# Kernel optimization log

Measured on AMD Instinct MI355X. Metric: run time of the kernel, lower is better.

The kernel has to match this reference:

```python
import jax, jax.numpy as jnp
import numpy as np

B, C, H, W = 16, 256, 56, 56
K = 7            # involution kernel size
GC = 16          # group_channels
G = C // GC      # groups = 16
RED = C // 4     # reduction_ratio = 4
EPS = 1e-5
PAD = (K - 1) // 2


def _bn(x, g, b, m, v):
    # eval-mode BatchNorm2d over channel dim of (B,C,H,W)
    scale = g / jnp.sqrt(v + EPS)
    return x * scale[:, None, None] + (b - m * scale)[:, None, None]


def _conv1x1(x, w, b):
    # x: (B,Cin,H,W), w: (Cout,Cin)
    return jnp.einsum('bchw,oc->bohw', x, w) + b[None, :, None, None]


def setup_inputs() -> dict:
    key = jax.random.key(0)
    ks = jax.random.split(key, 32)
    def n(i, shape, s=0.05):
        return jax.random.normal(ks[i], shape, jnp.float32) * s
    return {
        'x': jax.random.normal(ks[0], (B, C, H, W), jnp.float32),
        'w1': n(1, (C, C)), 'b1': n(2, (C,)),
        'bn1_g': 1.0 + n(3, (C,)), 'bn1_b': n(4, (C,)),
        'bn1_m': n(5, (C,)), 'bn1_v': 1.0 + 0.1 * jax.random.uniform(ks[6], (C,)),
        'red_w': n(7, (RED, C)), 'red_b': n(8, (RED,)),
        'red_bn_g': 1.0 + n(9, (RED,)), 'red_bn_b': n(10, (RED,)),
        'red_bn_m': n(11, (RED,)), 'red_bn_v': 1.0 + 0.1 * jax.random.uniform(ks[12], (RED,)),
        'span_w': n(13, (K * K * G, RED)), 'span_b': n(14, (K * K * G,)),
        'bn2_g': 1.0 + n(15, (C,)), 'bn2_b': n(16, (C,)),
        'bn2_m': n(17, (C,)), 'bn2_v': 1.0 + 0.1 * jax.random.uniform(ks[18], (C,)),
        'w3': n(19, (C, C)), 'b3': n(20, (C,)),
        'bn3_g': 1.0 + n(21, (C,)), 'bn3_b': n(22, (C,)),
        'bn3_m': n(23, (C,)), 'bn3_v': 1.0 + 0.1 * jax.random.uniform(ks[24], (C,)),
    }


def _involution(y, red_w, red_b, rg, rb, rm, rv, span_w, span_b):
    # dynamic per-pixel kernels: (B, G, K*K, H, W)
    r = jax.nn.relu(_bn(_conv1x1(y, red_w, red_b), rg, rb, rm, rv))
    wd = _conv1x1(r, span_w, span_b).reshape(B, G, K * K, H, W)
    # pad input once; accumulate over the K*K shifted views (no unfold copy)
    yp = jnp.pad(y, ((0, 0), (0, 0), (PAD, PAD), (PAD, PAD)))
    yp = yp.reshape(B, G, GC, H + 2 * PAD, W + 2 * PAD)
    out = jnp.zeros((B, G, GC, H, W), y.dtype)
    for i in range(K):
        for j in range(K):
            out = out + wd[:, :, i * K + j, None] * yp[:, :, :, i:i + H, j:j + W]
    return out.reshape(B, C, H, W)


def reference(x, w1, b1, bn1_g, bn1_b, bn1_m, bn1_v,
              red_w, red_b, red_bn_g, red_bn_b, red_bn_m, red_bn_v,
              span_w, span_b, bn2_g, bn2_b, bn2_m, bn2_v,
              w3, b3, bn3_g, bn3_b, bn3_m, bn3_v):
    y = jnp.tanh(_bn(_conv1x1(x, w1, b1), bn1_g, bn1_b, bn1_m, bn1_v))
    y = _involution(y, red_w, red_b, red_bn_g, red_bn_b, red_bn_m, red_bn_v, span_w, span_b)
    y = jnp.tanh(_bn(y, bn2_g, bn2_b, bn2_m, bn2_v))
    y = _bn(_conv1x1(y, w3, b3), bn3_g, bn3_b, bn3_m, bn3_v)
    return y + x  # use_skip: inv_stride==1 and input_dim==output_dim
```

## Files before the change

### kernel.cpp

```cpp
#include <hip/hip_runtime.h>
#include <math.h>

#define DEV_EPS 1e-5f

namespace {
constexpr int B_ = 16, C_ = 256, H_ = 56, W_ = 56, HW_ = H_ * W_;
constexpr int G_ = 16, GC_ = 16, RED_ = 64, KK_ = 49;
constexpr int NTOT = B_ * HW_;

typedef __attribute__((ext_vector_type(8))) short short8;
typedef __attribute__((ext_vector_type(4))) float f32x4;

__device__ __forceinline__ unsigned short bf16r(float f) {
  unsigned u = __float_as_uint(f);
  u += 0x7fff + ((u >> 16) & 1);
  return (unsigned short)(u >> 16);
}
__device__ __forceinline__ float bf2f(unsigned short s) {
  return __uint_as_float((unsigned)s << 16);
}

__device__ __forceinline__ float fast_tanh(float x) {
  float ax = fabsf(x);
  float e = __expf(-2.0f * ax);
  float r = (1.0f - e) * __builtin_amdgcn_rcpf(1.0f + e);
  return copysignf(r, x);
}

__device__ __forceinline__ void gl_lds16(const void* g, void* l) {
  __builtin_amdgcn_global_load_lds(
      (const __attribute__((address_space(1))) unsigned int*)g,
      (__attribute__((address_space(3))) unsigned int*)l, 16, 0, 0);
}

template <int WM, int WN, int KD, int EPI>
__global__ __launch_bounds__(256)
void mfma_gemm(const unsigned short* __restrict__ A,
               const unsigned short* __restrict__ Act,
               const float* __restrict__ p0,
               const float* __restrict__ bg, const float* __restrict__ bb,
               const float* __restrict__ bm, const float* __restrict__ bv,
               const float* __restrict__ xskip, void* __restrict__ outp,
               int M) {
  constexpr int BM = WM * 64, BN = WN * 64;
  __shared__ unsigned short At[BM * 64];
  __shared__ unsigned short Bt[BN * 64];
  __shared__ float aS[BM], bS[BM];

  const int tid = threadIdx.x;
  const int n0 = blockIdx.x * BN, m0 = blockIdx.y * BM;
  const int wave = tid >> 6, lane = tid & 63;
  const int wm = (WM == 2) ? (wave >> 1) : 0;
  const int wn = (WM == 2) ? (wave & 1) : wave;

  if (tid < BM) {
    int m = min(m0 + tid, M - 1);
    float sc = bg[m] * rsqrtf(bv[m] + DEV_EPS);
    aS[tid] = sc;
    bS[tid] = sc * p0[m] + bb[m] - bm[m] * sc;
  }

  f32x4 acc[4][4];
#pragma unroll
  for (int i = 0; i < 4; ++i)
#pragma unroll
    for (int j = 0; j < 4; ++j)
#pragma unroll
      for (int e = 0; e < 4; ++e) acc[i][j][e] = 0.f;

  const int lq = lane & 7;
  const int lr8 = lane >> 3;
  const int quad = lane >> 4, ln = lane & 15;

#pragma unroll 1
  for (int kt = 0; kt < KD / 64; ++kt) {
    __syncthreads();
#pragma unroll
    for (int t = 0; t < BM / 32; ++t) {
      int inst = wave * (BM / 32) + t;
      int row = inst * 8 + lr8;
      int mrow = min(m0 + row, M - 1);
      int qs = lq ^ (row & 7);
      gl_lds16(A + (size_t)mrow * KD + kt * 64 + qs * 8, &At[inst * 512]);
    }
#pragma unroll
    for (int t = 0; t < BN / 32; ++t) {
      int inst = wave * (BN / 32) + t;
      int row = inst * 8 + lr8;
      int qs = lq ^ (row & 7);
      gl_lds16(Act + (size_t)(n0 + row) * KD + kt * 64 + qs * 8, &Bt[inst * 512]);
    }
    __syncthreads();

#pragma unroll
    for (int s = 0; s < 2; ++s) {
      const int c = s * 4 + quad;
      short8 af[4], bf[4];
#pragma unroll
      for (int i = 0; i < 4; ++i) {
        int r = wm * 64 + i * 16 + ln;
        af[i] = *(const short8*)&At[r * 64 + (c ^ (r & 7)) * 8];
      }
#pragma unroll
      for (int j = 0; j < 4; ++j) {
        int r = wn * 64 + j * 16 + ln;
        bf[j] = *(const short8*)&Bt[r * 64 + (c ^ (r & 7)) * 8];
      }
#pragma unroll
      for (int i = 0; i < 4; ++i)
#pragma unroll
        for (int j = 0; j < 4; ++j)
          acc[i][j] = __builtin_amdgcn_mfma_f32_16x16x32_bf16(af[i], bf[j],
                                                              acc[i][j], 0, 0, 0);
    }
  }

#pragma unroll
  for (int i = 0; i < 4; ++i) {
    const int mloc = wm * 64 + i * 16 + quad * 4;
#pragma unroll
    for (int j = 0; j < 4; ++j) {
      const int np = n0 + wn * 64 + j * 16 + ln;
      if (EPI == 0 || EPI == 1) {
        ushort4 pk;
        unsigned short* pp = (unsigned short*)&pk;
#pragma unroll
        for (int r = 0; r < 4; ++r) {
          float v = aS[mloc + r] * acc[i][j][r] + bS[mloc + r];
          v = (EPI == 0) ? fast_tanh(v) : fmaxf(v, 0.f);
          pp[r] = bf16r(v);
        }
        *(ushort4*)((unsigned short*)outp + (size_t)np * M + m0 + mloc) = pk;
      } else {
        int b = np / HW_, hw = np - b * HW_;
        size_t base = ((size_t)b * C_ + m0 + mloc) * HW_ + hw;
#pragma unroll
        for (int r = 0; r < 4; ++r) {
          size_t o = base + (size_t)r * HW_;
          ((float*)outp)[o] =
              aS[mloc + r] * acc[i][j][r] + bS[mloc + r] + xskip[o];
        }
      }
    }
  }
}

constexpr int YS_STR = 264;

__global__ __launch_bounds__(256)
void gemm_yr(const unsigned short* __restrict__ A,
             const unsigned short* __restrict__ Act,
             const unsigned short* __restrict__ redw,
             const float* __restrict__ p0,
             const float* __restrict__ bg, const float* __restrict__ bb,
             const float* __restrict__ bm, const float* __restrict__ bv,
             const float* __restrict__ rp0,
             const float* __restrict__ rbg, const float* __restrict__ rbb,
             const float* __restrict__ rbm, const float* __restrict__ rbv,
             unsigned short* __restrict__ yT, unsigned short* __restrict__ rT) {
  constexpr int BM = 256, BN = 64;
  __shared__ __align__(16) unsigned short blob2[BM * 64 + BN * 64];
  __shared__ float aS[256], bS[256], aR[64], bR[64];
  unsigned short* At = blob2;
  unsigned short* Bt = blob2 + BM * 64;
  unsigned short* yS = blob2;

  const int tid = threadIdx.x;
  const int n0 = blockIdx.x * BN;
  const int wave = tid >> 6, lane = tid & 63;
  const int lq = lane & 7, lr8 = lane >> 3;
  const int quad = lane >> 4, ln = lane & 15;

  {
    float sc = bg[tid] * rsqrtf(bv[tid] + DEV_EPS);
    aS[tid] = sc;
    bS[tid] = sc * p0[tid] + bb[tid] - bm[tid] * sc;
    if (tid < 64) {
      float s2 = rbg[tid] * rsqrtf(rbv[tid] + DEV_EPS);
      aR[tid] = s2;
      bR[tid] = s2 * rp0[tid] + rbb[tid] - rbm[tid] * s2;
    }
  }

  f32x4 acc[4][4];
#pragma unroll
  for (int i = 0; i < 4; ++i)
#pragma unroll
    for (int j = 0; j < 4; ++j)
#pragma unroll
      for (int e = 0; e < 4; ++e) acc[i][j][e] = 0.f;

#pragma unroll 1
  for (int kt = 0; kt < 4; ++kt) {
    __syncthreads();
#pragma unroll
    for (int t = 0; t < 8; ++t) {
      int inst = wave * 8 + t;
      int row = inst * 8 + lr8;
      int qs = lq ^ (row & 7);
      gl_lds16(A + (size_t)row * 256 + kt * 64 + qs * 8, &At[inst * 512]);
    }
#pragma unroll
    for (int t = 0; t < 2; ++t) {
      int inst = wave * 2 + t;
      int row = inst * 8 + lr8;
      int qs = lq ^ (row & 7);
      gl_lds16(Act + (size_t)(n0 + row) * 256 + kt * 64 + qs * 8,
               &Bt[inst * 512]);
    }
    __syncthreads();

#pragma unroll
    for (int s = 0; s < 2; ++s) {
      const int c = s * 4 + quad;
      short8 af[4], bf[4];
#pragma unroll
      for (int i = 0; i < 4; ++i) {
        int r = wave * 64 + i * 16 + ln;
        af[i] = *(const short8*)&At[r * 64 + (c ^ (r & 7)) * 8];
      }
#pragma unroll
      for (int j = 0; j < 4; ++j) {
        int r = j * 16 + ln;
        bf[j] = *(const short8*)&Bt[r * 64 + (c ^ (r & 7)) * 8];
      }
#pragma unroll
      for (int i = 0; i < 4; ++i)
#pragma unroll
        for (int j = 0; j < 4; ++j)
          acc[i][j] = __builtin_amdgcn_mfma_f32_16x16x32_bf16(af[i], bf[j],
                                                              acc[i][j], 0, 0, 0);
    }
  }

  __syncthreads();

#pragma unroll
  for (int i = 0; i < 4; ++i) {
    const int mloc = wave * 64 + i * 16 + quad * 4;
#pragma unroll
    for (int j = 0; j < 4; ++j) {
      const int npl = j * 16 + ln;
      ushort4 pk;
      unsigned short* pp = (unsigned short*)&pk;
#pragma unroll
      for (int r = 0; r < 4; ++r) {
        float v = aS[mloc + r] * acc[i][j][r] + bS[mloc + r];
        pp[r] = bf16r(fast_tanh(v));
      }
      *(ushort4*)(yT + (size_t)(n0 + npl) * 256 + mloc) = pk;
      *(ushort4*)(yS + npl * YS_STR + mloc) = pk;
    }
  }
  __syncthreads();

  f32x4 acc2[4];
#pragma unroll
  for (int j = 0; j < 4; ++j)
#pragma unroll
    for (int e = 0; e < 4; ++e) acc2[j][e] = 0.f;
#pragma unroll
  for (int kc = 0; kc < 8; ++kc) {
    short8 af2 =
        *(const short8*)&redw[(size_t)(wave * 16 + ln) * 256 + kc * 32 + quad * 8];
#pragma unroll
    for (int j = 0; j < 4; ++j) {
      short8 bf2 = *(const short8*)&yS[(j * 16 + ln) * YS_STR + kc * 32 + quad * 8];
      acc2[j] = __builtin_amdgcn_mfma_f32_16x16x32_bf16(af2, bf2, acc2[j], 0, 0, 0);
    }
  }
  {
    const int m2 = wave * 16 + quad * 4;
#pragma unroll
    for (int j = 0; j < 4; ++j) {
      const int np = n0 + j * 16 + ln;
      ushort4 pk;
      unsigned short* pp = (unsigned short*)&pk;
#pragma unroll
      for (int r = 0; r < 4; ++r) {
        float v = aR[m2 + r] * acc2[j][r] + bR[m2 + r];
        pp[r] = bf16r(fmaxf(v, 0.f));
      }
      *(ushort4*)(rT + (size_t)np * 64 + m2) = pk;
    }
  }
}

__global__ __launch_bounds__(256)
void transpose_x(const float* __restrict__ x, unsigned short* __restrict__ xT) {
  __shared__ unsigned short tile[128 * 72];
  const int tid = threadIdx.x;
  const int px0 = blockIdx.x * 128;
  for (int p = 0; p < 4; ++p) {
    if (p) __syncthreads();
#pragma unroll
    for (int e = 0; e < 32; ++e) {
      int flat = e * 256 + tid;
      int cl = flat >> 7, pxl = flat & 127;
      int px = px0 + pxl;
      int b = px / HW_, hw = px - b * HW_;
      tile[pxl * 72 + cl] = bf16r(x[((size_t)b * C_ + p * 64 + cl) * HW_ + hw]);
    }
    __syncthreads();
    int px = tid >> 1, half = tid & 1;
    const unsigned short* src = &tile[px * 72 + half * 32];
    unsigned short* dst = &xT[(size_t)(px0 + px) * C_ + p * 64 + half * 32];
    *(uint4*)(dst + 0) = *(const uint4*)(src + 0);
    *(uint4*)(dst + 8) = *(const uint4*)(src + 8);
    *(uint4*)(dst + 16) = *(const uint4*)(src + 16);
    *(uint4*)(dst + 24) = *(const uint4*)(src + 24);
  }
}

__global__ __launch_bounds__(256)
void wconv(const float* __restrict__ w1, const float* __restrict__ rw,
           const float* __restrict__ sw, const float* __restrict__ w3,
           unsigned short* __restrict__ o1, unsigned short* __restrict__ orw,
           unsigned short* __restrict__ osw, unsigned short* __restrict__ ow3) {
  int i = blockIdx.x * 256 + threadIdx.x;
  if (i < 65536) o1[i] = bf16r(w1[i]);
  if (i < 16384) orw[i] = bf16r(rw[i]);
  if (i < 50176) osw[i] = bf16r(sw[i]);
  if (i < 65536) ow3[i] = bf16r(w3[i]);
}

constexpr int PB_STR = 648;
constexpr int W_TAP_STR = 232;
constexpr int BLOB_N = 25320;

__global__ __launch_bounds__(256)
void gather_inv(const unsigned short* __restrict__ yT,
                const unsigned short* __restrict__ rT,
                const unsigned short* __restrict__ spanw,
                const float* __restrict__ spanb,
                const float* __restrict__ g2, const float* __restrict__ b2,
                const float* __restrict__ m2, const float* __restrict__ v2,
                unsigned short* __restrict__ tT) {
  __shared__ __align__(16) unsigned short blob[BLOB_N];
  __shared__ float a2s[16], b2s[16], sbs[KK_];

  unsigned short* rs = blob;
  unsigned short* sws = blob + 14336;
  unsigned short* patchb = blob;
  unsigned short* wts = blob + 10368;
  unsigned short* tb = blob + 21736;

  const int tid = threadIdx.x;
  const int g = blockIdx.x;
  const int st = blockIdx.y;
  const int b = blockIdx.z;
  const int h0 = st * 4;
  const int wave = tid >> 6, lane = tid & 63;
  const int lq = lane & 7, lr8 = lane >> 3;
  const int quad = lane >> 4, ln = lane & 15;

  uint4 pv0[3], pv1[3];
  int poff[3];
  bool pok[3];
#pragma unroll
  for (int pi = 0; pi < 3; ++pi) {
    int e = tid + pi * 256;
    bool ok = e < 620;
    int row = e / 62, cw = e - row * 62;
    int sr = h0 + row - 3, sc = cw - 3;
    poff[pi] = row * 64 + cw;
    pok[pi] = ok;
    bool inb = ok && sr >= 0 && sr < H_ && sc >= 0 && sc < W_;
    if (inb) {
      const unsigned short* yp =
          yT + ((size_t)b * HW_ + sr * W_ + sc) * C_ + g * GC_;
      pv0[pi] = *(const uint4*)yp;
      pv1[pi] = *(const uint4*)(yp + 8);
    } else {
      pv0[pi] = make_uint4(0, 0, 0, 0);
      pv1[pi] = make_uint4(0, 0, 0, 0);
    }
  }

  {
    const unsigned short* rbase = rT + ((size_t)b * HW_ + h0 * W_) * RED_;
#pragma unroll
    for (int t = 0; t < 7; ++t) {
      int inst = wave * 7 + t;
      int row = inst * 8 + lr8;
      int qs = lq ^ (row & 7);
      gl_lds16(rbase + (size_t)row * RED_ + qs * 8, &rs[inst * 512]);
    }
    const unsigned short* swg = spanw + (size_t)(g * KK_) * RED_;
#pragma unroll
    for (int t = 0; t < 2; ++t) {
      int inst = wave * 2 + t;
      int row = inst * 8 + lr8;
      int tap = min(row, KK_ - 1);
      int qs = lq ^ (row & 7);
      gl_lds16(swg + (size_t)tap * RED_ + qs * 8, &sws[inst * 512]);
    }
    if (tid < 16) {
      int c = g * GC_ + tid;
      float sc = g2[c] * rsqrtf(v2[c] + DEV_EPS);
      a2s[tid] = sc;
      b2s[tid] = b2[c] - m2[c] * sc;
    }
    if (tid < KK_) sbs[tid] = spanb[g * KK_ + tid];
  }
  __syncthreads();

  f32x4 wacc[14];
#pragma unroll
  for (int j = 0; j < 14; ++j)
#pragma unroll
    for (int e = 0; e < 4; ++e) wacc[j][e] = 0.f;
  {
    short8 af[2];
#pragma unroll
    for (int s = 0; s < 2; ++s) {
      int c = s * 4 + quad;
      int r = wave * 16 + ln;
      af[s] = *(const short8*)&sws[r * 64 + (c ^ (r & 7)) * 8];
    }
#pragma unroll
    for (int j = 0; j < 14; ++j) {
#pragma unroll
      for (int s = 0; s < 2; ++s) {
        int c = s * 4 + quad;
        int r = j * 16 + ln;
        short8 bf = *(const short8*)&rs[r * 64 + (c ^ (r & 7)) * 8];
        wacc[j] = __builtin_amdgcn_mfma_f32_16x16x32_bf16(af[s], bf, wacc[j],
                                                          0, 0, 0);
      }
    }
  }
  __syncthreads();

  {
#pragma unroll
    for (int r = 0; r < 4; ++r) {
      int tap = wave * 16 + quad * 4 + r;
      if (tap < KK_) {
        float sb = sbs[tap];
#pragma unroll
        for (int j = 0; j < 14; ++j)
          wts[tap * W_TAP_STR + j * 16 + ln] = bf16r(wacc[j][r] + sb);
      }
    }
#pragma unroll
    for (int pi = 0; pi < 3; ++pi) {
      if (pok[pi]) {
        int off = poff[pi];
        unsigned wv[8] = {pv0[pi].x, pv0[pi].y, pv0[pi].z, pv0[pi].w,
                          pv1[pi].x, pv1[pi].y, pv1[pi].z, pv1[pi].w};
#pragma unroll
        for (int cc = 0; cc < 8; ++cc) {
          patchb[(2 * cc) * PB_STR + off] = (unsigned short)wv[cc];
          patchb[(2 * cc + 1) * PB_STR + off] = (unsigned short)(wv[cc] >> 16);
        }
      }
    }
  }
  __syncthreads();

#pragma unroll 1
  for (int it = 0; it < 2; ++it) {
    int item = tid + it * 256;
    if (item < 56 * 8) {
      const int gcp = item & 7, s = item >> 3;
      const int gc0 = gcp * 2;
      const int r0 = s / 14, c0 = (s - r0 * 14) * 4;
      const unsigned short* pg0 = patchb + gc0 * PB_STR + r0 * 64 + c0;
      const unsigned short* pg1 = pg0 + PB_STR;
      const unsigned short* wp = wts + (r0 * 56 + c0);
      float a00 = 0.f, a01 = 0.f, a02 = 0.f, a03 = 0.f;
      float a10 = 0.f, a11 = 0.f, a12 = 0.f, a13 = 0.f;
#pragma unroll
      for (int di = 0; di < 7; ++di) {
        const unsigned short* p0p = pg0 + di * 64;
        const unsigned short* p1p = pg1 + di * 64;
        uint2 q0 = *(const uint2*)p0p;
        uint2 q1 = *(const uint2*)(p0p + 4);
        uint2 q2 = *(const uint2*)(p0p + 8);
        uint2 u0 = *(const uint2*)p1p;
        uint2 u1 = *(const uint2*)(p1p + 4);
        uint2 u2 = *(const uint2*)(p1p + 8);
        unsigned uu0[6] = {q0.x, q0.y, q1.x, q1.y, q2.x, q2.y};
        unsigned uu1[6] = {u0.x, u0.y, u1.x, u1.y, u2.x, u2.y};
        float pf0[12], pf1[12];
#pragma unroll
        for (int k = 0; k < 6; ++k) {
          pf0[2 * k] = __uint_as_float(uu0[k] << 16);
          pf0[2 * k + 1] = __uint_as_float(uu0[k] & 0xffff0000u);
          pf1[2 * k] = __uint_as_float(uu1[k] << 16);
          pf1[2 * k + 1] = __uint_as_float(uu1[k] & 0xffff0000u);
        }
#pragma unroll
        for (int dj = 0; dj < 7; ++dj) {
          ushort4 wv = *(const ushort4*)(wp + (di * 7 + dj) * W_TAP_STR);
          float w0 = bf2f(wv.x), w1 = bf2f(wv.y), w2 = bf2f(wv.z),
                w3 = bf2f(wv.w);
          a00 += w0 * pf0[dj + 0];
          a01 += w1 * pf0[dj + 1];
          a02 += w2 * pf0[dj + 2];
          a03 += w3 * pf0[dj + 3];
          a10 += w0 * pf1[dj + 0];
          a11 += w1 * pf1[dj + 1];
          a12 += w2 * pf1[dj + 2];
          a13 += w3 * pf1[dj + 3];
        }
      }
      const int pxb = r0 * 56 + c0;
      {
        const float al = a2s[gc0], be = b2s[gc0];
        tb[(pxb + 0) * 16 + gc0] = bf16r(fast_tanh(al * a00 + be));
        tb[(pxb + 1) * 16 + gc0] = bf16r(fast_tanh(al * a01 + be));
        tb[(pxb + 2) * 16 + gc0] = bf16r(fast_tanh(al * a02 + be));
        tb[(pxb + 3) * 16 + gc0] = bf16r(fast_tanh(al * a03 + be));
      }
      {
        const float al = a2s[gc0 + 1], be = b2s[gc0 + 1];
        tb[(pxb + 0) * 16 + gc0 + 1] = bf16r(fast_tanh(al * a10 + be));
        tb[(pxb + 1) * 16 + gc0 + 1] = bf16r(fast_tanh(al * a11 + be));
        tb[(pxb + 2) * 16 + gc0 + 1] = bf16r(fast_tanh(al * a12 + be));
        tb[(pxb + 3) * 16 + gc0 + 1] = bf16r(fast_tanh(al * a13 + be));
      }
    }
  }
  __syncthreads();

  if (tid < 224) {
    unsigned short* dst = tT + ((size_t)b * HW_ + h0 * W_ + tid) * C_ + g * GC_;
    *(uint4*)(dst + 0) = *(const uint4*)&tb[tid * 16];
    *(uint4*)(dst + 8) = *(const uint4*)&tb[tid * 16 + 8];
  }
}

}

extern "C" void kernel_launch(void* const* d_in, const int* in_sizes, int n_in,
                              void* d_out, int out_size, void* d_ws, size_t ws_size,
                              hipStream_t stream) {
  const float* x = (const float*)d_in[0];
  const float* w1 = (const float*)d_in[1];
  const float* b1 = (const float*)d_in[2];
  const float* bn1g = (const float*)d_in[3];
  const float* bn1b = (const float*)d_in[4];
  const float* bn1m = (const float*)d_in[5];
  const float* bn1v = (const float*)d_in[6];
  const float* red_w = (const float*)d_in[7];
  const float* red_b = (const float*)d_in[8];
  const float* rbg = (const float*)d_in[9];
  const float* rbb = (const float*)d_in[10];
  const float* rbm = (const float*)d_in[11];
  const float* rbv = (const float*)d_in[12];
  const float* span_w = (const float*)d_in[13];
  const float* span_b = (const float*)d_in[14];
  const float* bn2g = (const float*)d_in[15];
  const float* bn2b = (const float*)d_in[16];
  const float* bn2m = (const float*)d_in[17];
  const float* bn2v = (const float*)d_in[18];
  const float* w3 = (const float*)d_in[19];
  const float* b3 = (const float*)d_in[20];
  const float* bn3g = (const float*)d_in[21];
  const float* bn3b = (const float*)d_in[22];
  const float* bn3m = (const float*)d_in[23];
  const float* bn3v = (const float*)d_in[24];

  unsigned short* ws = (unsigned short*)d_ws;
  unsigned short* xT = ws;
  unsigned short* yT = xT + (size_t)NTOT * C_;
  unsigned short* rT = yT + (size_t)NTOT * C_;
  unsigned short* tT = rT + (size_t)NTOT * RED_;
  unsigned short* w1b = tT + (size_t)NTOT * C_;
  unsigned short* redb = w1b + 65536;
  unsigned short* spanb = redb + 16384;
  unsigned short* w3b = spanb + 50176;
  float* out = (float*)d_out;

  dim3 blk(256);
  wconv<<<dim3(256), blk, 0, stream>>>(w1, red_w, span_w, w3, w1b, redb, spanb, w3b);
  transpose_x<<<dim3(392), blk, 0, stream>>>(x, xT);
  gemm_yr<<<dim3(784), blk, 0, stream>>>(
      w1b, xT, redb, b1, bn1g, bn1b, bn1m, bn1v,
      red_b, rbg, rbb, rbm, rbv, yT, rT);
  gather_inv<<<dim3(16, 14, 16), blk, 0, stream>>>(
      yT, rT, spanb, span_b, bn2g, bn2b, bn2m, bn2v, tT);
  mfma_gemm<2, 2, 256, 3><<<dim3(392, 2), blk, 0, stream>>>(
      w3b, tT, b3, bn3g, bn3b, bn3m, bn3v, x, out, C_);
}
```

Before: 311.4 us.

## Fuse x transpose into first GEMM and double-buffer activation tiles

New measurement: 271.4 us. 1.15x faster.

```diff
diff --git a/kernel.cpp b/kernel.cpp
--- a/kernel.cpp
+++ b/kernel.cpp
@@ -33,123 +33,11 @@
       (__attribute__((address_space(3))) unsigned int*)l, 16, 0, 0);
 }
 
-template <int WM, int WN, int KD, int EPI>
-__global__ __launch_bounds__(256)
-void mfma_gemm(const unsigned short* __restrict__ A,
-               const unsigned short* __restrict__ Act,
-               const float* __restrict__ p0,
-               const float* __restrict__ bg, const float* __restrict__ bb,
-               const float* __restrict__ bm, const float* __restrict__ bv,
-               const float* __restrict__ xskip, void* __restrict__ outp,
-               int M) {
-  constexpr int BM = WM * 64, BN = WN * 64;
-  __shared__ unsigned short At[BM * 64];
-  __shared__ unsigned short Bt[BN * 64];
-  __shared__ float aS[BM], bS[BM];
-
-  const int tid = threadIdx.x;
-  const int n0 = blockIdx.x * BN, m0 = blockIdx.y * BM;
-  const int wave = tid >> 6, lane = tid & 63;
-  const int wm = (WM == 2) ? (wave >> 1) : 0;
-  const int wn = (WM == 2) ? (wave & 1) : wave;
-
-  if (tid < BM) {
-    int m = min(m0 + tid, M - 1);
-    float sc = bg[m] * rsqrtf(bv[m] + DEV_EPS);
-    aS[tid] = sc;
-    bS[tid] = sc * p0[m] + bb[m] - bm[m] * sc;
-  }
-
-  f32x4 acc[4][4];
-#pragma unroll
-  for (int i = 0; i < 4; ++i)
-#pragma unroll
-    for (int j = 0; j < 4; ++j)
-#pragma unroll
-      for (int e = 0; e < 4; ++e) acc[i][j][e] = 0.f;
-
-  const int lq = lane & 7;
-  const int lr8 = lane >> 3;
-  const int quad = lane >> 4, ln = lane & 15;
-
-#pragma unroll 1
-  for (int kt = 0; kt < KD / 64; ++kt) {
-    __syncthreads();
-#pragma unroll
-    for (int t = 0; t < BM / 32; ++t) {
-      int inst = wave * (BM / 32) + t;
-      int row = inst * 8 + lr8;
-      int mrow = min(m0 + row, M - 1);
-      int qs = lq ^ (row & 7);
-      gl_lds16(A + (size_t)mrow * KD + kt * 64 + qs * 8, &At[inst * 512]);
-    }
-#pragma unroll
-    for (int t = 0; t < BN / 32; ++t) {
-      int inst = wave * (BN / 32) + t;
-      int row = inst * 8 + lr8;
-      int qs = lq ^ (row & 7);
-      gl_lds16(Act + (size_t)(n0 + row) * KD + kt * 64 + qs * 8, &Bt[inst * 512]);
-    }
-    __syncthreads();
-
-#pragma unroll
-    for (int s = 0; s < 2; ++s) {
-      const int c = s * 4 + quad;
-      short8 af[4], bf[4];
-#pragma unroll
-      for (int i = 0; i < 4; ++i) {
-        int r = wm * 64 + i * 16 + ln;
-        af[i] = *(const short8*)&At[r * 64 + (c ^ (r & 7)) * 8];
-      }
-#pragma unroll
-      for (int j = 0; j < 4; ++j) {
-        int r = wn * 64 + j * 16 + ln;
-        bf[j] = *(const short8*)&Bt[r * 64 + (c ^ (r & 7)) * 8];
-      }
-#pragma unroll
-      for (int i = 0; i < 4; ++i)
-#pragma unroll
-        for (int j = 0; j < 4; ++j)
-          acc[i][j] = __builtin_amdgcn_mfma_f32_16x16x32_bf16(af[i], bf[j],
-                                                              acc[i][j], 0, 0, 0);
-    }
-  }
-
-#pragma unroll
-  for (int i = 0; i < 4; ++i) {
-    const int mloc = wm * 64 + i * 16 + quad * 4;
-#pragma unroll
-    for (int j = 0; j < 4; ++j) {
-      const int np = n0 + wn * 64 + j * 16 + ln;
-      if (EPI == 0 || EPI == 1) {
-        ushort4 pk;
-        unsigned short* pp = (unsigned short*)&pk;
-#pragma unroll
-        for (int r = 0; r < 4; ++r) {
-          float v = aS[mloc + r] * acc[i][j][r] + bS[mloc + r];
-          v = (EPI == 0) ? fast_tanh(v) : fmaxf(v, 0.f);
-          pp[r] = bf16r(v);
-        }
-        *(ushort4*)((unsigned short*)outp + (size_t)np * M + m0 + mloc) = pk;
-      } else {
-        int b = np / HW_, hw = np - b * HW_;
-        size_t base = ((size_t)b * C_ + m0 + mloc) * HW_ + hw;
-#pragma unroll
-        for (int r = 0; r < 4; ++r) {
-          size_t o = base + (size_t)r * HW_;
-          ((float*)outp)[o] =
-              aS[mloc + r] * acc[i][j][r] + bS[mloc + r] + xskip[o];
-        }
-      }
-    }
-  }
-}
-
 constexpr int YS_STR = 264;
 
 __global__ __launch_bounds__(256)
 void gemm_yr(const unsigned short* __restrict__ A,
-             const unsigned short* __restrict__ Act,
+             const float* __restrict__ x,
              const unsigned short* __restrict__ redw,
              const float* __restrict__ p0,
              const float* __restrict__ bg, const float* __restrict__ bb,
@@ -158,18 +46,18 @@
              const float* __restrict__ rbg, const float* __restrict__ rbb,
              const float* __restrict__ rbm, const float* __restrict__ rbv,
              unsigned short* __restrict__ yT, unsigned short* __restrict__ rT) {
-  constexpr int BM = 256, BN = 64;
-  __shared__ __align__(16) unsigned short blob2[BM * 64 + BN * 64];
+  __shared__ __align__(16) unsigned short blob2[16896];
   __shared__ float aS[256], bS[256], aR[64], bR[64];
-  unsigned short* At = blob2;
-  unsigned short* Bt = blob2 + BM * 64;
+  unsigned short* Bt0 = blob2;
+  unsigned short* Bt1 = blob2 + 4096;
   unsigned short* yS = blob2;
 
   const int tid = threadIdx.x;
-  const int n0 = blockIdx.x * BN;
+  const int n0 = blockIdx.x * 64;
+  const int bi = n0 / HW_, hw0 = n0 - bi * HW_;
   const int wave = tid >> 6, lane = tid & 63;
-  const int lq = lane & 7, lr8 = lane >> 3;
   const int quad = lane >> 4, ln = lane & 15;
+  const int c2 = tid >> 3, pxo = tid & 7;
 
   {
     float sc = bg[tid] * rsqrtf(bv[tid] + DEV_EPS);
@@ -182,6 +70,28 @@
     }
   }
 
+  float4 xa, xb, xc, xd;
+  auto load_x = [&](int kt) {
+    const float* p = x + ((size_t)bi * C_ + kt * 64 + 2 * c2) * HW_ + hw0 + pxo * 8;
+    xa = *(const float4*)p;
+    xb = *(const float4*)(p + 4);
+    xc = *(const float4*)(p + HW_);
+    xd = *(const float4*)(p + HW_ + 4);
+  };
+  auto commit_x = [&](unsigned short* bt) {
+    float e0[8] = {xa.x, xa.y, xa.z, xa.w, xb.x, xb.y, xb.z, xb.w};
+    float e1[8] = {xc.x, xc.y, xc.z, xc.w, xd.x, xd.y, xd.z, xd.w};
+    const int kc = c2 >> 2;
+    const int off = 2 * (c2 & 3);
+#pragma unroll
+    for (int i = 0; i < 8; ++i) {
+      int pxl = pxo * 8 + i;
+      int slot = kc ^ (i & 7);
+      unsigned pk = (unsigned)bf16r(e0[i]) | ((unsigned)bf16r(e1[i]) << 16);
+      *(unsigned*)&bt[pxl * 64 + slot * 8 + off] = pk;
+    }
+  };
+
   f32x4 acc[4][4];
 #pragma unroll
   for (int i = 0; i < 4; ++i)
@@ -189,40 +99,28 @@
     for (int j = 0; j < 4; ++j)
 #pragma unroll
       for (int e = 0; e < 4; ++e) acc[i][j][e] = 0.f;
+
+  load_x(0);
+  commit_x(Bt0);
+  __syncthreads();
 
 #pragma unroll 1
   for (int kt = 0; kt < 4; ++kt) {
-    __syncthreads();
-#pragma unroll
-    for (int t = 0; t < 8; ++t) {
-      int inst = wave * 8 + t;
-      int row = inst * 8 + lr8;
-      int qs = lq ^ (row & 7);
-      gl_lds16(A + (size_t)row * 256 + kt * 64 + qs * 8, &At[inst * 512]);
-    }
-#pragma unroll
-    for (int t = 0; t < 2; ++t) {
-      int inst = wave * 2 + t;
-      int row = inst * 8 + lr8;
-      int qs = lq ^ (row & 7);
-      gl_lds16(Act + (size_t)(n0 + row) * 256 + kt * 64 + qs * 8,
-               &Bt[inst * 512]);
-    }
-    __syncthreads();
-
+    unsigned short* cur = (kt & 1) ? Bt1 : Bt0;
+    unsigned short* nxt = (kt & 1) ? Bt0 : Bt1;
+    if (kt < 3) load_x(kt + 1);
 #pragma unroll
     for (int s = 0; s < 2; ++s) {
       const int c = s * 4 + quad;
       short8 af[4], bf[4];
 #pragma unroll
-      for (int i = 0; i < 4; ++i) {
-        int r = wave * 64 + i * 16 + ln;
-        af[i] = *(const short8*)&At[r * 64 + (c ^ (r & 7)) * 8];
-      }
+      for (int i = 0; i < 4; ++i)
+        af[i] = *(const short8*)&A[(size_t)(wave * 64 + i * 16 + ln) * 256 +
+                                   kt * 64 + c * 8];
 #pragma unroll
       for (int j = 0; j < 4; ++j) {
         int r = j * 16 + ln;
-        bf[j] = *(const short8*)&Bt[r * 64 + (c ^ (r & 7)) * 8];
+        bf[j] = *(const short8*)&cur[r * 64 + (c ^ (r & 7)) * 8];
       }
 #pragma unroll
       for (int i = 0; i < 4; ++i)
@@ -231,9 +129,9 @@
           acc[i][j] = __builtin_amdgcn_mfma_f32_16x16x32_bf16(af[i], bf[j],
                                                               acc[i][j], 0, 0, 0);
     }
-  }
-
-  __syncthreads();
+    if (kt < 3) commit_x(nxt);
+    __syncthreads();
+  }
 
 #pragma unroll
   for (int i = 0; i < 4; ++i) {
@@ -287,28 +185,96 @@
 }
 
 __global__ __launch_bounds__(256)
-void transpose_x(const float* __restrict__ x, unsigned short* __restrict__ xT) {
-  __shared__ unsigned short tile[128 * 72];
+void gemm_out(const unsigned short* __restrict__ A,
+              const unsigned short* __restrict__ Act,
+              const float* __restrict__ p0,
+              const float* __restrict__ bg, const float* __restrict__ bb,
+              const float* __restrict__ bm, const float* __restrict__ bv,
+              const float* __restrict__ xskip, float* __restrict__ out) {
+  __shared__ __align__(16) unsigned short Bt[2][128 * 64];
+  __shared__ float aS[128], bS[128];
+
   const int tid = threadIdx.x;
-  const int px0 = blockIdx.x * 128;
-  for (int p = 0; p < 4; ++p) {
-    if (p) __syncthreads();
-#pragma unroll
-    for (int e = 0; e < 32; ++e) {
-      int flat = e * 256 + tid;
-      int cl = flat >> 7, pxl = flat & 127;
-      int px = px0 + pxl;
-      int b = px / HW_, hw = px - b * HW_;
-      tile[pxl * 72 + cl] = bf16r(x[((size_t)b * C_ + p * 64 + cl) * HW_ + hw]);
+  const int n0 = blockIdx.x * 128, m0 = blockIdx.y * 128;
+  const int wave = tid >> 6, lane = tid & 63;
+  const int wm = wave >> 1, wn = wave & 1;
+  const int lq = lane & 7, lr8 = lane >> 3;
+  const int quad = lane >> 4, ln = lane & 15;
+
+  if (tid < 128) {
+    int m = m0 + tid;
+    float sc = bg[m] * rsqrtf(bv[m] + DEV_EPS);
+    aS[tid] = sc;
+    bS[tid] = sc * p0[m] + bb[m] - bm[m] * sc;
+  }
+
+  f32x4 acc[4][4];
+#pragma unroll
+  for (int i = 0; i < 4; ++i)
+#pragma unroll
+    for (int j = 0; j < 4; ++j)
+#pragma unroll
+      for (int e = 0; e < 4; ++e) acc[i][j][e] = 0.f;
+
+#pragma unroll
+  for (int t = 0; t < 4; ++t) {
+    int inst = wave * 4 + t;
+    int row = inst * 8 + lr8;
+    int qs = lq ^ (row & 7);
+    gl_lds16(Act + (size_t)(n0 + row) * 256 + qs * 8, &Bt[0][inst * 512]);
+  }
+  __syncthreads();
+
+#pragma unroll 1
+  for (int kt = 0; kt < 4; ++kt) {
+    const int cur = kt & 1;
+    if (kt < 3) {
+#pragma unroll
+      for (int t = 0; t < 4; ++t) {
+        int inst = wave * 4 + t;
+        int row = inst * 8 + lr8;
+        int qs = lq ^ (row & 7);
+        gl_lds16(Act + (size_t)(n0 + row) * 256 + (kt + 1) * 64 + qs * 8,
+                 &Bt[cur ^ 1][inst * 512]);
+      }
+    }
+#pragma unroll
+    for (int s = 0; s < 2; ++s) {
+      const int c = s * 4 + quad;
+      short8 af[4], bf[4];
+#pragma unroll
+      for (int i = 0; i < 4; ++i)
+        af[i] = *(const short8*)&A[(size_t)(m0 + wm * 64 + i * 16 + ln) * 256 +
+                                   kt * 64 + c * 8];
+#pragma unroll
+      for (int j = 0; j < 4; ++j) {
+        int r = wn * 64 + j * 16 + ln;
+        bf[j] = *(const short8*)&Bt[cur][r * 64 + (c ^ (r & 7)) * 8];
+      }
+#pragma unroll
+      for (int i = 0; i < 4; ++i)
+#pragma unroll
+        for (int j = 0; j < 4; ++j)
+          acc[i][j] = __builtin_amdgcn_mfma_f32_16x16x32_bf16(af[i], bf[j],
+                                                              acc[i][j], 0, 0, 0);
     }
     __syncthreads();
-    int px = tid >> 1, half = tid & 1;
-    const unsigned short* src = &tile[px * 72 + half * 32];
-    unsigned short* dst = &xT[(size_t)(px0 + px) * C_ + p * 64 + half * 32];
-    *(uint4*)(dst + 0) = *(const uint4*)(src + 0);
-    *(uint4*)(dst + 8) = *(const uint4*)(src + 8);
-    *(uint4*)(dst + 16) = *(const uint4*)(src + 16);
-    *(uint4*)(dst + 24) = *(const uint4*)(src + 24);
+  }
+
+#pragma unroll
+  for (int i = 0; i < 4; ++i) {
+    const int mloc = wm * 64 + i * 16 + quad * 4;
+#pragma unroll
+    for (int j = 0; j < 4; ++j) {
+      const int np = n0 + wn * 64 + j * 16 + ln;
+      int b = np / HW_, hw = np - b * HW_;
+      size_t base = ((size_t)b * C_ + m0 + mloc) * HW_ + hw;
+#pragma unroll
+      for (int r = 0; r < 4; ++r) {
+        size_t o = base + (size_t)r * HW_;
+        out[o] = aS[mloc + r] * acc[i][j][r] + bS[mloc + r] + xskip[o];
+      }
+    }
   }
 }
 
@@ -573,15 +539,15 @@
   unsigned short* spanb = redb + 16384;
   unsigned short* w3b = spanb + 50176;
   float* out = (float*)d_out;
+  (void)xT;
 
   dim3 blk(256);
   wconv<<<dim3(256), blk, 0, stream>>>(w1, red_w, span_w, w3, w1b, redb, spanb, w3b);
-  transpose_x<<<dim3(392), blk, 0, stream>>>(x, xT);
   gemm_yr<<<dim3(784), blk, 0, stream>>>(
-      w1b, xT, redb, b1, bn1g, bn1b, bn1m, bn1v,
+      w1b, x, redb, b1, bn1g, bn1b, bn1m, bn1v,
       red_b, rbg, rbb, rbm, rbv, yT, rT);
   gather_inv<<<dim3(16, 14, 16), blk, 0, stream>>>(
       yT, rT, spanb, span_b, bn2g, bn2b, bn2m, bn2v, tT);
-  mfma_gemm<2, 2, 256, 3><<<dim3(392, 2), blk, 0, stream>>>(
-      w3b, tT, b3, bn3g, bn3b, bn3m, bn3v, x, out, C_);
-}
+  gemm_out<<<dim3(392, 2), blk, 0, stream>>>(
+      w3b, tT, b3, bn3g, bn3b, bn3m, bn3v, x, out);
+}
```
